# Optimization experiments

Measured on AMD Instinct MI355X. Metric: run time of the kernel, lower is better.

The kernel has to match this reference:

```python
import jax, jax.numpy as jnp
import numpy as np

B, LQ, LK = 4, 256, 512
DQ = DK = PROJ = 256


def setup_inputs() -> dict:
    key = jax.random.key(0)
    ks = jax.random.split(key, 8)
    query = jax.random.normal(ks[0], (B, LQ, DQ), dtype=jnp.float32)
    keys = jax.random.normal(ks[1], (B, LK, DK), dtype=jnp.float32)
    attn_mask = jax.random.bernoulli(ks[2], 0.1, (B, LQ, LK))
    # Linear(query_size+key_size, proj) split into query/key halves (same math as concat @ W1)
    s1 = 1.0 / np.sqrt(DQ + DK)
    Wq = jax.random.uniform(ks[3], (DQ, PROJ), jnp.float32, -s1, s1)
    Wk = jax.random.uniform(ks[4], (DK, PROJ), jnp.float32, -s1, s1)
    b1 = jax.random.uniform(ks[5], (PROJ,), jnp.float32, -s1, s1)
    s2 = 1.0 / np.sqrt(PROJ)
    w2 = jax.random.uniform(ks[6], (PROJ,), jnp.float32, -s2, s2)
    b2 = jax.random.uniform(ks[7], (), jnp.float32, -s2, s2)
    return {"query": query, "keys": keys, "attn_mask": attn_mask,
            "Wq": Wq, "Wk": Wk, "b1": b1, "w2": w2, "b2": b2}


def reference(query, keys, attn_mask, Wq, Wk, b1, w2, b2):
    # cat(q_expand, k_expand) @ W1 == q@Wq broadcast-added to k@Wk (avoids the huge concat)
    qp = jnp.einsum('bqd,dp->bqp', query, Wq)            # (B,Lq,P)
    kp = jnp.einsum('bkd,dp->bkp', keys, Wk)             # (B,Lk,P)
    h = jnp.tanh(qp[:, :, None, :] + kp[:, None, :, :] + b1)  # (B,Lq,Lk,P)
    logits = jnp.einsum('bqkp,p->bqk', h, w2) + b2        # (B,Lq,Lk)
    logits = jnp.where(attn_mask, -jnp.inf, logits)
    return logits
```

## Files before the change

kernel.cpp:

```cpp
#include <hip/hip_runtime.h>
#include <math.h>

#define B_ 4
#define LQ_ 256
#define LK_ 512
#define D_ 256
#define P_ 256

#define SC 2.8853900817779268f

#define MASK_SENTINEL (-3.0e38f)

__global__ __launch_bounds__(256) void proj_kernel(
    const float* __restrict__ Q, const float* __restrict__ Kx,
    const float* __restrict__ Wq, const float* __restrict__ Wk,
    const float* __restrict__ b1,
    float* __restrict__ Eq, float* __restrict__ Ek)
{
    __shared__ __align__(16) float Ws[256][68];

    const int bm = blockIdx.x;
    const int bn = blockIdx.y;
    const bool isq = (bm < 32);
    const int m0 = isq ? bm * 32 : (bm - 32) * 32;
    const float* A = isq ? Q : Kx;
    const float* W = isq ? Wq : Wk;
    float* outp    = isq ? Eq : Ek;
    const int n0 = bn * 64;

    const int t  = threadIdx.x;
    const int tx = t & 15;
    const int ty = t >> 4;

    #pragma unroll
    for (int i = 0; i < 16; ++i) {
        int f  = t + i * 256;
        int r  = f >> 4;
        int c4 = (f & 15) * 4;
        *(float4*)&Ws[r][c4] = *(const float4*)&W[(size_t)r * P_ + n0 + c4];
    }
    __syncthreads();

    const float* arow0 = A + (size_t)(m0 + ty) * D_;
    const float* arow1 = A + (size_t)(m0 + ty + 16) * D_;

    float acc[2][4] = {};

    float4 a0c = *(const float4*)&arow0[0];
    float4 a1c = *(const float4*)&arow1[0];
    float4 w0c = *(const float4*)&Ws[0][tx * 4];
    float4 w1c = *(const float4*)&Ws[1][tx * 4];
    float4 w2c = *(const float4*)&Ws[2][tx * 4];
    float4 w3c = *(const float4*)&Ws[3][tx * 4];

    #pragma unroll 4
    for (int k4 = 0; k4 < 64; ++k4) {
        float4 a0 = a0c, a1 = a1c, w0 = w0c, w1 = w1c, w2v = w2c, w3 = w3c;
        if (k4 < 63) {
            a0c = *(const float4*)&arow0[(k4 + 1) * 4];
            a1c = *(const float4*)&arow1[(k4 + 1) * 4];
            w0c = *(const float4*)&Ws[k4 * 4 + 4][tx * 4];
            w1c = *(const float4*)&Ws[k4 * 4 + 5][tx * 4];
            w2c = *(const float4*)&Ws[k4 * 4 + 6][tx * 4];
            w3c = *(const float4*)&Ws[k4 * 4 + 7][tx * 4];
        }
        float av[2][4] = {{a0.x,a0.y,a0.z,a0.w},{a1.x,a1.y,a1.z,a1.w}};
        float wv[4][4] = {{w0.x,w0.y,w0.z,w0.w},{w1.x,w1.y,w1.z,w1.w},
                          {w2v.x,w2v.y,w2v.z,w2v.w},{w3.x,w3.y,w3.z,w3.w}};
        #pragma unroll
        for (int kk = 0; kk < 4; ++kk)
            #pragma unroll
            for (int i = 0; i < 2; ++i)
                #pragma unroll
                for (int j = 0; j < 4; ++j)
                    acc[i][j] = fmaf(av[i][kk], wv[kk][j], acc[i][j]);
    }

    float bv[4] = {0.f, 0.f, 0.f, 0.f};
    if (!isq) {
        float4 b = *(const float4*)&b1[n0 + tx * 4];
        bv[0] = b.x; bv[1] = b.y; bv[2] = b.z; bv[3] = b.w;
    }

    #pragma unroll
    for (int i = 0; i < 2; ++i) {
        int m = m0 + ty + i * 16;
        float4 o;
        o.x = __builtin_amdgcn_exp2f(SC * (acc[i][0] + bv[0]));
        o.y = __builtin_amdgcn_exp2f(SC * (acc[i][1] + bv[1]));
        o.z = __builtin_amdgcn_exp2f(SC * (acc[i][2] + bv[2]));
        o.w = __builtin_amdgcn_exp2f(SC * (acc[i][3] + bv[3]));
        *(float4*)&outp[(size_t)m * P_ + n0 + tx * 4] = o;
    }
}

__global__ __launch_bounds__(256) void logits_kernel(
    const float* __restrict__ Eq, const float* __restrict__ Ek,
    const unsigned char* __restrict__ mask,
    const float* __restrict__ w2, const float* __restrict__ b2,
    float* __restrict__ out)
{
    __shared__ __align__(16) float eqs[32][260];
    __shared__ __align__(16) float eks[32][260];
    __shared__ float partial[4];

    const int b  = blockIdx.z;
    const int q0 = blockIdx.y * 32;
    const int k0 = blockIdx.x * 32;
    const int t  = threadIdx.x;

    #pragma unroll
    for (int i = 0; i < 8; ++i) {
        int f = t + i * 256;
        int r = f >> 6;
        int c = (f & 63) * 4;
        *(float4*)&eqs[r][c] = *(const float4*)&Eq[(size_t)(b * LQ_ + q0 + r) * P_ + c];
        *(float4*)&eks[r][c] = *(const float4*)&Ek[(size_t)(b * LK_ + k0 + r) * P_ + c];
    }
    float wv = w2[t];
    #pragma unroll
    for (int s = 32; s > 0; s >>= 1) wv += __shfl_xor(wv, s);
    if ((t & 63) == 0) partial[t >> 6] = wv;
    __syncthreads();

    const float base = partial[0] + partial[1] + partial[2] + partial[3] + b2[0];

    const int tx = t & 15;
    const int ty = t >> 4;

    size_t oidx[2][2];
    unsigned char mb[2][2];
    #pragma unroll
    for (int i = 0; i < 2; ++i)
        #pragma unroll
        for (int j = 0; j < 2; ++j) {
            oidx[i][j] = (size_t)(b * LQ_ + q0 + ty + i * 16) * LK_ + (k0 + tx + j * 16);
            mb[i][j] = mask[oidx[i][j]];
        }

    const float* q0p = &eqs[ty][0];
    const float* q1p = &eqs[ty + 16][0];
    const float* k0p = &eks[tx][0];
    const float* k1p = &eks[tx + 16][0];

    float acc[2][2] = {};

    #pragma unroll 4
    for (int p4 = 0; p4 < 64; ++p4) {
        const float4 w = *(const float4*)&w2[p4 * 4];
        float4 qv[2], kv[2];
        qv[0] = *(const float4*)(q0p + p4 * 4);
        qv[1] = *(const float4*)(q1p + p4 * 4);
        kv[0] = *(const float4*)(k0p + p4 * 4);
        kv[1] = *(const float4*)(k1p + p4 * 4);
        float qa[2][4] = {{qv[0].x,qv[0].y,qv[0].z,qv[0].w},
                          {qv[1].x,qv[1].y,qv[1].z,qv[1].w}};
        float ka[2][4] = {{kv[0].x,kv[0].y,kv[0].z,kv[0].w},
                          {kv[1].x,kv[1].y,kv[1].z,kv[1].w}};
        #pragma unroll
        for (int i = 0; i < 2; ++i)
            #pragma unroll
            for (int j = 0; j < 2; ++j) {
                float x0 = fmaf(qa[i][0], ka[j][0], 1.f);
                float x1 = fmaf(qa[i][1], ka[j][1], 1.f);
                float x2 = fmaf(qa[i][2], ka[j][2], 1.f);
                float x3 = fmaf(qa[i][3], ka[j][3], 1.f);
                float d01 = x0 * x1;
                float d23 = x2 * x3;
                float n01 = fmaf(w.x, x1, w.y * x0);
                float n23 = fmaf(w.z, x3, w.w * x2);
                acc[i][j] = fmaf(fmaf(n01, d23, n23 * d01),
                                 __builtin_amdgcn_rcpf(d01 * d23),
                                 acc[i][j]);
            }
    }

    #pragma unroll
    for (int i = 0; i < 2; ++i)
        #pragma unroll
        for (int j = 0; j < 2; ++j)
            out[oidx[i][j]] = mb[i][j] ? MASK_SENTINEL : fmaf(-2.f, acc[i][j], base);
}

extern "C" void kernel_launch(void* const* d_in, const int* in_sizes, int n_in,
                              void* d_out, int out_size, void* d_ws, size_t ws_size,
                              hipStream_t stream) {
    const float* query        = (const float*)d_in[0];
    const float* keys         = (const float*)d_in[1];
    const unsigned char* mask = (const unsigned char*)d_in[2];
    const float* Wq           = (const float*)d_in[3];
    const float* Wk           = (const float*)d_in[4];
    const float* b1           = (const float*)d_in[5];
    const float* w2           = (const float*)d_in[6];
    const float* b2           = (const float*)d_in[7];
    float* out = (float*)d_out;

    float* Eq = (float*)d_ws;
    float* Ek = Eq + (size_t)B_ * LQ_ * P_;

    dim3 g1(96, 4);
    proj_kernel<<<g1, 256, 0, stream>>>(query, keys, Wq, Wk, b1, Eq, Ek);

    dim3 g2(LK_ / 32, LQ_ / 32, B_);
    logits_kernel<<<g2, 256, 0, stream>>>(Eq, Ek, mask, w2, b2, out);
}
```

Measured before the change: 32.60 us.

## Fuse projection and logits kernels into one persistent launch with grid barrier

Merges the projection and logits kernels into a single 512-block launch. The first 384 blocks compute the exp-projections, then every block meets at a global atomic-counter barrier before computing its logits tile. The aim is to remove the second kernel launch and the inter-kernel gap. In exchange it adds a memset launch and a spin-wait barrier, and it relies on all 512 blocks being resident at once (launch_bounds 256,2 across 256 CUs) to avoid deadlock.

```diff
diff --git a/kernel.cpp b/kernel.cpp
--- a/kernel.cpp
+++ b/kernel.cpp
@@ -11,175 +11,186 @@
 
 #define MASK_SENTINEL (-3.0e38f)
 
-__global__ __launch_bounds__(256) void proj_kernel(
+#define NBLOCKS 512u
+
+__global__ __launch_bounds__(256, 2) void fused_kernel(
     const float* __restrict__ Q, const float* __restrict__ Kx,
     const float* __restrict__ Wq, const float* __restrict__ Wk,
-    const float* __restrict__ b1,
-    float* __restrict__ Eq, float* __restrict__ Ek)
+    const float* __restrict__ b1, const unsigned char* __restrict__ mask,
+    const float* __restrict__ w2, const float* __restrict__ b2,
+    float* __restrict__ Eq, float* __restrict__ Ek,
+    unsigned int* __restrict__ ctr, float* __restrict__ out)
 {
-    __shared__ __align__(16) float Ws[256][68];
-
-    const int bm = blockIdx.x;
-    const int bn = blockIdx.y;
-    const bool isq = (bm < 32);
-    const int m0 = isq ? bm * 32 : (bm - 32) * 32;
-    const float* A = isq ? Q : Kx;
-    const float* W = isq ? Wq : Wk;
-    float* outp    = isq ? Eq : Ek;
-    const int n0 = bn * 64;
-
+    __shared__ __align__(16) float lds[17408];
+    __shared__ float partial[4];
+
+    const int wg = blockIdx.x;
     const int t  = threadIdx.x;
     const int tx = t & 15;
     const int ty = t >> 4;
 
-    #pragma unroll
-    for (int i = 0; i < 16; ++i) {
-        int f  = t + i * 256;
-        int r  = f >> 4;
-        int c4 = (f & 15) * 4;
-        *(float4*)&Ws[r][c4] = *(const float4*)&W[(size_t)r * P_ + n0 + c4];
+    if (wg < 384) {
+        float (*Ws)[68] = (float(*)[68])lds;
+
+        const int bm = wg >> 2;
+        const int bn = wg & 3;
+        const bool isq = (bm < 32);
+        const int m0 = isq ? bm * 32 : (bm - 32) * 32;
+        const float* A = isq ? Q : Kx;
+        const float* W = isq ? Wq : Wk;
+        float* outp    = isq ? Eq : Ek;
+        const int n0 = bn * 64;
+
+        #pragma unroll
+        for (int i = 0; i < 16; ++i) {
+            int f  = t + i * 256;
+            int r  = f >> 4;
+            int c4 = (f & 15) * 4;
+            *(float4*)&Ws[r][c4] = *(const float4*)&W[(size_t)r * P_ + n0 + c4];
+        }
+        __syncthreads();
+
+        const float* arow0 = A + (size_t)(m0 + ty) * D_;
+        const float* arow1 = A + (size_t)(m0 + ty + 16) * D_;
+
+        float acc[2][4] = {};
+
+        float4 a0c = *(const float4*)&arow0[0];
+        float4 a1c = *(const float4*)&arow1[0];
+        float4 u0c = *(const float4*)&Ws[0][tx * 4];
+        float4 u1c = *(const float4*)&Ws[1][tx * 4];
+        float4 u2c = *(const float4*)&Ws[2][tx * 4];
+        float4 u3c = *(const float4*)&Ws[3][tx * 4];
+
+        #pragma unroll 4
+        for (int k4 = 0; k4 < 64; ++k4) {
+            float4 a0 = a0c, a1 = a1c, u0 = u0c, u1 = u1c, u2 = u2c, u3 = u3c;
+            if (k4 < 63) {
+                a0c = *(const float4*)&arow0[(k4 + 1) * 4];
+                a1c = *(const float4*)&arow1[(k4 + 1) * 4];
+                u0c = *(const float4*)&Ws[k4 * 4 + 4][tx * 4];
+                u1c = *(const float4*)&Ws[k4 * 4 + 5][tx * 4];
+                u2c = *(const float4*)&Ws[k4 * 4 + 6][tx * 4];
+                u3c = *(const float4*)&Ws[k4 * 4 + 7][tx * 4];
+            }
+            float av[2][4] = {{a0.x,a0.y,a0.z,a0.w},{a1.x,a1.y,a1.z,a1.w}};
+            float wv[4][4] = {{u0.x,u0.y,u0.z,u0.w},{u1.x,u1.y,u1.z,u1.w},
+                              {u2.x,u2.y,u2.z,u2.w},{u3.x,u3.y,u3.z,u3.w}};
+            #pragma unroll
+            for (int kk = 0; kk < 4; ++kk)
+                #pragma unroll
+                for (int i = 0; i < 2; ++i)
+                    #pragma unroll
+                    for (int j = 0; j < 4; ++j)
+                        acc[i][j] = fmaf(av[i][kk], wv[kk][j], acc[i][j]);
+        }
+
+        float bv[4] = {0.f, 0.f, 0.f, 0.f};
+        if (!isq) {
+            float4 b = *(const float4*)&b1[n0 + tx * 4];
+            bv[0] = b.x; bv[1] = b.y; bv[2] = b.z; bv[3] = b.w;
+        }
+
+        #pragma unroll
+        for (int i = 0; i < 2; ++i) {
+            int m = m0 + ty + i * 16;
+            float4 o;
+            o.x = __builtin_amdgcn_exp2f(SC * (acc[i][0] + bv[0]));
+            o.y = __builtin_amdgcn_exp2f(SC * (acc[i][1] + bv[1]));
+            o.z = __builtin_amdgcn_exp2f(SC * (acc[i][2] + bv[2]));
+            o.w = __builtin_amdgcn_exp2f(SC * (acc[i][3] + bv[3]));
+            *(float4*)&outp[(size_t)m * P_ + n0 + tx * 4] = o;
+        }
+    }
+
+    __syncthreads();
+    if (t == 0) {
+        __hip_atomic_fetch_add(ctr, 1u, __ATOMIC_RELEASE, __HIP_MEMORY_SCOPE_AGENT);
+        while (__hip_atomic_load(ctr, __ATOMIC_ACQUIRE, __HIP_MEMORY_SCOPE_AGENT) < NBLOCKS) {
+            __builtin_amdgcn_s_sleep(8);
+        }
     }
     __syncthreads();
 
-    const float* arow0 = A + (size_t)(m0 + ty) * D_;
-    const float* arow1 = A + (size_t)(m0 + ty + 16) * D_;
-
-    float acc[2][4] = {};
-
-    float4 a0c = *(const float4*)&arow0[0];
-    float4 a1c = *(const float4*)&arow1[0];
-    float4 w0c = *(const float4*)&Ws[0][tx * 4];
-    float4 w1c = *(const float4*)&Ws[1][tx * 4];
-    float4 w2c = *(const float4*)&Ws[2][tx * 4];
-    float4 w3c = *(const float4*)&Ws[3][tx * 4];
-
-    #pragma unroll 4
-    for (int k4 = 0; k4 < 64; ++k4) {
-        float4 a0 = a0c, a1 = a1c, w0 = w0c, w1 = w1c, w2v = w2c, w3 = w3c;
-        if (k4 < 63) {
-            a0c = *(const float4*)&arow0[(k4 + 1) * 4];
-            a1c = *(const float4*)&arow1[(k4 + 1) * 4];
-            w0c = *(const float4*)&Ws[k4 * 4 + 4][tx * 4];
-            w1c = *(const float4*)&Ws[k4 * 4 + 5][tx * 4];
-            w2c = *(const float4*)&Ws[k4 * 4 + 6][tx * 4];
-            w3c = *(const float4*)&Ws[k4 * 4 + 7][tx * 4];
-        }
-        float av[2][4] = {{a0.x,a0.y,a0.z,a0.w},{a1.x,a1.y,a1.z,a1.w}};
-        float wv[4][4] = {{w0.x,w0.y,w0.z,w0.w},{w1.x,w1.y,w1.z,w1.w},
-                          {w2v.x,w2v.y,w2v.z,w2v.w},{w3.x,w3.y,w3.z,w3.w}};
-        #pragma unroll
-        for (int kk = 0; kk < 4; ++kk)
+    {
+        float (*eqs)[260] = (float(*)[260])lds;
+        float (*eks)[260] = (float(*)[260])(lds + 32 * 260);
+
+        const int kt = wg & 15;
+        const int qt = (wg >> 4) & 7;
+        const int b  = wg >> 7;
+        const int q0 = qt * 32;
+        const int k0 = kt * 32;
+
+        #pragma unroll
+        for (int i = 0; i < 8; ++i) {
+            int f = t + i * 256;
+            int r = f >> 6;
+            int c = (f & 63) * 4;
+            *(float4*)&eqs[r][c] = *(const float4*)&Eq[(size_t)(b * LQ_ + q0 + r) * P_ + c];
+            *(float4*)&eks[r][c] = *(const float4*)&Ek[(size_t)(b * LK_ + k0 + r) * P_ + c];
+        }
+        float wv = w2[t];
+        #pragma unroll
+        for (int s = 32; s > 0; s >>= 1) wv += __shfl_xor(wv, s);
+        if ((t & 63) == 0) partial[t >> 6] = wv;
+        __syncthreads();
+
+        const float base = partial[0] + partial[1] + partial[2] + partial[3] + b2[0];
+
+        size_t oidx[2][2];
+        unsigned char mb[2][2];
+        #pragma unroll
+        for (int i = 0; i < 2; ++i)
+            #pragma unroll
+            for (int j = 0; j < 2; ++j) {
+                oidx[i][j] = (size_t)(b * LQ_ + q0 + ty + i * 16) * LK_ + (k0 + tx + j * 16);
+                mb[i][j] = mask[oidx[i][j]];
+            }
+
+        const float* q0p = &eqs[ty][0];
+        const float* q1p = &eqs[ty + 16][0];
+        const float* k0p = &eks[tx][0];
+        const float* k1p = &eks[tx + 16][0];
+
+        float acc[2][2] = {};
+
+        #pragma unroll 4
+        for (int p4 = 0; p4 < 64; ++p4) {
+            const float4 w = *(const float4*)&w2[p4 * 4];
+            float4 qv[2], kv[2];
+            qv[0] = *(const float4*)(q0p + p4 * 4);
+            qv[1] = *(const float4*)(q1p + p4 * 4);
+            kv[0] = *(const float4*)(k0p + p4 * 4);
+            kv[1] = *(const float4*)(k1p + p4 * 4);
+            float qa[2][4] = {{qv[0].x,qv[0].y,qv[0].z,qv[0].w},
+                              {qv[1].x,qv[1].y,qv[1].z,qv[1].w}};
+            float ka[2][4] = {{kv[0].x,kv[0].y,kv[0].z,kv[0].w},
+                              {kv[1].x,kv[1].y,kv[1].z,kv[1].w}};
             #pragma unroll
             for (int i = 0; i < 2; ++i)
                 #pragma unroll
-                for (int j = 0; j < 4; ++j)
-                    acc[i][j] = fmaf(av[i][kk], wv[kk][j], acc[i][j]);
+                for (int j = 0; j < 2; ++j) {
+                    float x0 = fmaf(qa[i][0], ka[j][0], 1.f);
+                    float x1 = fmaf(qa[i][1], ka[j][1], 1.f);
+                    float x2 = fmaf(qa[i][2], ka[j][2], 1.f);
+                    float x3 = fmaf(qa[i][3], ka[j][3], 1.f);
+                    float d01 = x0 * x1;
+                    float d23 = x2 * x3;
+                    float n01 = fmaf(w.x, x1, w.y * x0);
+                    float n23 = fmaf(w.z, x3, w.w * x2);
+                    acc[i][j] = fmaf(fmaf(n01, d23, n23 * d01),
+                                     __builtin_amdgcn_rcpf(d01 * d23),
+                                     acc[i][j]);
+                }
+        }
+
+        #pragma unroll
+        for (int i = 0; i < 2; ++i)
+            #pragma unroll
+            for (int j = 0; j < 2; ++j)
+                out[oidx[i][j]] = mb[i][j] ? MASK_SENTINEL : fmaf(-2.f, acc[i][j], base);
     }
-
-    float bv[4] = {0.f, 0.f, 0.f, 0.f};
-    if (!isq) {
-        float4 b = *(const float4*)&b1[n0 + tx * 4];
-        bv[0] = b.x; bv[1] = b.y; bv[2] = b.z; bv[3] = b.w;
-    }
-
-    #pragma unroll
-    for (int i = 0; i < 2; ++i) {
-        int m = m0 + ty + i * 16;
-        float4 o;
-        o.x = __builtin_amdgcn_exp2f(SC * (acc[i][0] + bv[0]));
-        o.y = __builtin_amdgcn_exp2f(SC * (acc[i][1] + bv[1]));
-        o.z = __builtin_amdgcn_exp2f(SC * (acc[i][2] + bv[2]));
-        o.w = __builtin_amdgcn_exp2f(SC * (acc[i][3] + bv[3]));
-        *(float4*)&outp[(size_t)m * P_ + n0 + tx * 4] = o;
-    }
-}
-
-__global__ __launch_bounds__(256) void logits_kernel(
-    const float* __restrict__ Eq, const float* __restrict__ Ek,
-    const unsigned char* __restrict__ mask,
-    const float* __restrict__ w2, const float* __restrict__ b2,
-    float* __restrict__ out)
-{
-    __shared__ __align__(16) float eqs[32][260];
-    __shared__ __align__(16) float eks[32][260];
-    __shared__ float partial[4];
-
-    const int b  = blockIdx.z;
-    const int q0 = blockIdx.y * 32;
-    const int k0 = blockIdx.x * 32;
-    const int t  = threadIdx.x;
-
-    #pragma unroll
-    for (int i = 0; i < 8; ++i) {
-        int f = t + i * 256;
-        int r = f >> 6;
-        int c = (f & 63) * 4;
-        *(float4*)&eqs[r][c] = *(const float4*)&Eq[(size_t)(b * LQ_ + q0 + r) * P_ + c];
-        *(float4*)&eks[r][c] = *(const float4*)&Ek[(size_t)(b * LK_ + k0 + r) * P_ + c];
-    }
-    float wv = w2[t];
-    #pragma unroll
-    for (int s = 32; s > 0; s >>= 1) wv += __shfl_xor(wv, s);
-    if ((t & 63) == 0) partial[t >> 6] = wv;
-    __syncthreads();
-
-    const float base = partial[0] + partial[1] + partial[2] + partial[3] + b2[0];
-
-    const int tx = t & 15;
-    const int ty = t >> 4;
-
-    size_t oidx[2][2];
-    unsigned char mb[2][2];
-    #pragma unroll
-    for (int i = 0; i < 2; ++i)
-        #pragma unroll
-        for (int j = 0; j < 2; ++j) {
-            oidx[i][j] = (size_t)(b * LQ_ + q0 + ty + i * 16) * LK_ + (k0 + tx + j * 16);
-            mb[i][j] = mask[oidx[i][j]];
-        }
-
-    const float* q0p = &eqs[ty][0];
-    const float* q1p = &eqs[ty + 16][0];
-    const float* k0p = &eks[tx][0];
-    const float* k1p = &eks[tx + 16][0];
-
-    float acc[2][2] = {};
-
-    #pragma unroll 4
-    for (int p4 = 0; p4 < 64; ++p4) {
-        const float4 w = *(const float4*)&w2[p4 * 4];
-        float4 qv[2], kv[2];
-        qv[0] = *(const float4*)(q0p + p4 * 4);
-        qv[1] = *(const float4*)(q1p + p4 * 4);
-        kv[0] = *(const float4*)(k0p + p4 * 4);
-        kv[1] = *(const float4*)(k1p + p4 * 4);
-        float qa[2][4] = {{qv[0].x,qv[0].y,qv[0].z,qv[0].w},
-                          {qv[1].x,qv[1].y,qv[1].z,qv[1].w}};
-        float ka[2][4] = {{kv[0].x,kv[0].y,kv[0].z,kv[0].w},
-                          {kv[1].x,kv[1].y,kv[1].z,kv[1].w}};
-        #pragma unroll
-        for (int i = 0; i < 2; ++i)
-            #pragma unroll
-            for (int j = 0; j < 2; ++j) {
-                float x0 = fmaf(qa[i][0], ka[j][0], 1.f);
-                float x1 = fmaf(qa[i][1], ka[j][1], 1.f);
-                float x2 = fmaf(qa[i][2], ka[j][2], 1.f);
-                float x3 = fmaf(qa[i][3], ka[j][3], 1.f);
-                float d01 = x0 * x1;
-                float d23 = x2 * x3;
-                float n01 = fmaf(w.x, x1, w.y * x0);
-                float n23 = fmaf(w.z, x3, w.w * x2);
-                acc[i][j] = fmaf(fmaf(n01, d23, n23 * d01),
-                                 __builtin_amdgcn_rcpf(d01 * d23),
-                                 acc[i][j]);
-            }
-    }
-
-    #pragma unroll
-    for (int i = 0; i < 2; ++i)
-        #pragma unroll
-        for (int j = 0; j < 2; ++j)
-            out[oidx[i][j]] = mb[i][j] ? MASK_SENTINEL : fmaf(-2.f, acc[i][j], base);
 }
 
 extern "C" void kernel_launch(void* const* d_in, const int* in_sizes, int n_in,
@@ -197,10 +208,10 @@
 
     float* Eq = (float*)d_ws;
     float* Ek = Eq + (size_t)B_ * LQ_ * P_;
-
-    dim3 g1(96, 4);
-    proj_kernel<<<g1, 256, 0, stream>>>(query, keys, Wq, Wk, b1, Eq, Ek);
-
-    dim3 g2(LK_ / 32, LQ_ / 32, B_);
-    logits_kernel<<<g2, 256, 0, stream>>>(Eq, Ek, mask, w2, b2, out);
+    unsigned int* ctr = (unsigned int*)(Ek + (size_t)B_ * LK_ * P_);
+
+    hipMemsetAsync(ctr, 0, sizeof(unsigned int), stream);
+
+    fused_kernel<<<NBLOCKS, 256, 0, stream>>>(query, keys, Wq, Wk, b1, mask,
+                                              w2, b2, Eq, Ek, ctr, out);
 }
```

After: 97.00 us. 198% more time.
